# Optimization experiments

Hardware: AMD Instinct MI355X
Metric: run time of the kernel (lower is better)

## Reference

```python
import jax, jax.numpy as jnp
import numpy as np

POSE_DIM, H_DIM, LATENT_DIM, NUM_LAYERS = 96, 32, 16, 2
BATCH, OBS_LEN, PRED_LEN = 16384, 16, 25


def setup_inputs() -> dict:
    key = jax.random.key(0)
    ks = jax.random.split(key, 16)
    s = 0.1
    inp = {
        "obs_s": jax.random.normal(ks[0], (OBS_LEN, BATCH, POSE_DIM), jnp.float32),
        "latent": jax.random.normal(ks[1], (BATCH, LATENT_DIM), jnp.float32),
        "pred_len": PRED_LEN,
        # FC: latent_dim -> h_dim
        "W_fc": jax.random.normal(ks[2], (H_DIM, LATENT_DIM), jnp.float32) * s,
        "b_fc": jnp.zeros((H_DIM,), jnp.float32),
        # LSTM layer 0 (input pose_dim), PyTorch gate order i,f,g,o
        "W_ih0": jax.random.normal(ks[3], (4 * H_DIM, POSE_DIM), jnp.float32) * s,
        "W_hh0": jax.random.normal(ks[4], (4 * H_DIM, H_DIM), jnp.float32) * s,
        "b_ih0": jax.random.normal(ks[5], (4 * H_DIM,), jnp.float32) * s,
        "b_hh0": jax.random.normal(ks[6], (4 * H_DIM,), jnp.float32) * s,
        # LSTM layer 1 (input h_dim)
        "W_ih1": jax.random.normal(ks[7], (4 * H_DIM, H_DIM), jnp.float32) * s,
        "W_hh1": jax.random.normal(ks[8], (4 * H_DIM, H_DIM), jnp.float32) * s,
        "b_ih1": jax.random.normal(ks[9], (4 * H_DIM,), jnp.float32) * s,
        "b_hh1": jax.random.normal(ks[10], (4 * H_DIM,), jnp.float32) * s,
        # mlp: h_dim -> pose_dim
        "W_mlp": jax.random.normal(ks[11], (POSE_DIM, H_DIM), jnp.float32) * s,
        "b_mlp": jnp.zeros((POSE_DIM,), jnp.float32),
    }
    return inp


def _lstm_cell(x, h, c, W_ih, W_hh, b):
    # x: [B, in], h/c: [B, H]; gates in PyTorch order i, f, g, o
    gates = x @ W_ih.T + h @ W_hh.T + b
    i, f, g, o = jnp.split(gates, 4, axis=-1)
    c_new = jax.nn.sigmoid(f) * c + jax.nn.sigmoid(i) * jnp.tanh(g)
    h_new = jax.nn.sigmoid(o) * jnp.tanh(c_new)
    return h_new, c_new


def reference(obs_s, latent, pred_len, W_fc, b_fc,
              W_ih0, W_hh0, b_ih0, b_hh0,
              W_ih1, W_hh1, b_ih1, b_hh1,
              W_mlp, b_mlp):
    batch = obs_s.shape[1]
    h_init = latent @ W_fc.T + b_fc                    # [B, H] -> both layers
    c0 = jnp.zeros((batch, H_DIM), obs_s.dtype)
    b0 = b_ih0 + b_hh0
    b1 = b_ih1 + b_hh1

    def step(carry, _):
        last, h0, c0_, h1, c1_ = carry
        h0, c0_ = _lstm_cell(last, h0, c0_, W_ih0, W_hh0, b0)
        h1, c1_ = _lstm_cell(h0, h1, c1_, W_ih1, W_hh1, b1)
        curr = h1 @ W_mlp.T + b_mlp                    # [B, pose_dim]
        return (curr, h0, c0_, h1, c1_), curr

    init = (obs_s[-1], h_init, c0, h_init, c0)
    _, preds = jax.lax.scan(step, init, None, length=pred_len)
    return preds  # [pred_len, B, pose_dim]
```

## Files before the change

### kernel.cpp

```cpp
#include <hip/hip_runtime.h>


#define PRED 25
#define BATCH 16384
#define ET    32
#define XROW  192
#define HROW  128
#define LROW  64

typedef unsigned short u16;
typedef unsigned int   u32;
typedef __attribute__((ext_vector_type(8))) short bf16x8;
typedef __attribute__((ext_vector_type(4))) float f32x4;

#define LOG2E  1.44269504088896340736f
#define LOG2E2 2.88539008177792681472f

#define BARRIER_NOVM() asm volatile("s_waitcnt lgkmcnt(0)\ns_barrier" ::: "memory")

__device__ __forceinline__ float rcp_(float x){ return __builtin_amdgcn_rcpf(x); }
__device__ __forceinline__ float ex2(float x){ return __builtin_amdgcn_exp2f(x); }
__device__ __forceinline__ float sigm2(float xp){ return rcp_(1.0f + ex2(-xp)); }
__device__ __forceinline__ float tanh2(float xp){ return 1.0f - 2.0f*rcp_(ex2(xp) + 1.0f); }

__device__ __forceinline__ u16 f2b(float f){
  u32 i = __float_as_uint(f);
  i += 0x7FFFu + ((i >> 16) & 1u);
  return (u16)(i >> 16);
}
__device__ __forceinline__ float b2f(u16 u){ return __uint_as_float(((u32)u) << 16); }

struct __align__(16) SM {
  u16 xh[2][16*XROW];
  u16 hh[2][16*HROW];
  u16 h1lo[2][16*LROW];
};

__device__ __forceinline__ int swx(int e, int k){ return e*XROW + (k ^ ((e&7)<<3)); }
__device__ __forceinline__ int swh(int e, int k){ return e*HROW + (k ^ ((e&7)<<3)); }
__device__ __forceinline__ int swl(int e, int k){ return e*LROW + (k ^ ((e&7)<<3)); }

__device__ __forceinline__ bf16x8 pack8s(const float* src, float s){
  union { bf16x8 v; u16 h[8]; } fr;
  #pragma unroll
  for (int j = 0; j < 8; ++j) fr.h[j] = f2b(src[j]*s);
  return fr.v;
}

extern "C" __global__ __launch_bounds__(128, 1)
void decoder_kernel(const float* __restrict__ obs,  const float* __restrict__ lat,
                    const float* __restrict__ Wfc,  const float* __restrict__ bfc,
                    const float* __restrict__ Wih0, const float* __restrict__ Whh0,
                    const float* __restrict__ bih0, const float* __restrict__ bhh0,
                    const float* __restrict__ Wih1, const float* __restrict__ Whh1,
                    const float* __restrict__ bih1, const float* __restrict__ bhh1,
                    const float* __restrict__ Wmlp, const float* __restrict__ bmlp,
                    float* __restrict__ out)
{
  __shared__ SM sm;
  const int tid = threadIdx.x;
  const int ebase = blockIdx.x * ET;
  const int mh = tid >> 6;
  const int l  = tid & 63;
  const int lr = l & 15;
  const int kq = l >> 4;

  {
    int e = tid >> 2, c0 = (tid & 3)*24;
    int s = e >> 4, er = e & 15;
    const float* src = obs + ((size_t)(15*BATCH) + ebase + e)*96 + c0;
    #pragma unroll
    for (int j = 0; j < 12; ++j){
      float2 v = *(const float2*)(src + 2*j);
      u32 pk = (u32)f2b(v.x) | ((u32)f2b(v.y) << 16);
      *(u32*)&sm.xh[s][swx(er, c0 + 2*j)] = pk;
    }
  }
  {
    int u = tid & 31, e8 = (tid >> 5)*8;
    const float* wf = Wfc + u*16;
    float bb = bfc[u];
    #pragma unroll
    for (int r = 0; r < 8; ++r){
      int e = e8 + r, s = e >> 4, er = e & 15;
      const float* lp = lat + (size_t)(ebase + e)*16;
      float a = bb;
      #pragma unroll
      for (int j = 0; j < 16; ++j) a = fmaf(wf[j], lp[j], a);
      u16 hb = f2b(a);
      sm.xh[s][swx(er, 96 + u)] = hb;
      sm.hh[s][swh(er, 32 + u)] = hb;
    }
  }

  bf16x8 aw0[4][4];
  #pragma unroll
  for (int i = 0; i < 4; ++i){
    int vg = (mh*4 + i)*16 + lr;
    int g  = (vg & 3)*32 + (vg >> 2);
    float sc = ((vg & 3) == 2) ? LOG2E2 : LOG2E;
    #pragma unroll
    for (int c = 0; c < 4; ++c){
      int k = c*32 + kq*8;
      const float* src = (k < 96) ? (Wih0 + g*96 + k) : (Whh0 + g*32 + (k - 96));
      aw0[i][c] = pack8s(src, sc);
    }
  }
  bf16x8 aw1[4][2];
  #pragma unroll
  for (int i = 0; i < 4; ++i){
    int vg = (mh*4 + i)*16 + lr;
    int g  = (vg & 3)*32 + (vg >> 2);
    float sc = ((vg & 3) == 2) ? LOG2E2 : LOG2E;
    #pragma unroll
    for (int c = 0; c < 2; ++c){
      int k = c*32 + kq*8;
      const float* src = (k < 32) ? (Wih1 + g*32 + k) : (Whh1 + g*32 + (k - 32));
      aw1[i][c] = pack8s(src, sc);
    }
  }
  bf16x8 awm[3];
  #pragma unroll
  for (int i = 0; i < 3; ++i){
    int o = (mh*3 + i)*16 + lr;
    awm[i] = pack8s(Wmlp + o*32 + kq*8, 1.0f);
  }

  f32x4 bias0v[4], bias1v[4];
  #pragma unroll
  for (int i = 0; i < 4; ++i){
    int u = (mh*4 + i)*4 + kq;
    #pragma unroll
    for (int r = 0; r < 4; ++r){
      int g = r*32 + u;
      float sc = (r == 2) ? LOG2E2 : LOG2E;
      bias0v[i][r] = (bih0[g] + bhh0[g])*sc;
      bias1v[i][r] = (bih1[g] + bhh1[g])*sc;
    }
  }
  f32x4 biasmv[3];
  #pragma unroll
  for (int i = 0; i < 3; ++i){
    int o0 = (mh*3 + i)*16 + kq*4;
    #pragma unroll
    for (int r = 0; r < 4; ++r) biasmv[i][r] = bmlp[o0 + r];
  }

  float c0s[2][4] = {{0,0,0,0},{0,0,0,0}};
  float c1s[2][4] = {{0,0,0,0},{0,0,0,0}};

  __syncthreads();

  f32x4 am[2][3];

  for (int t = 0; t < PRED; ++t){
    const int p = t & 1;
    f32x4 g0[2][4];
    #pragma unroll
    for (int s = 0; s < 2; ++s){
      bf16x8 bx0 = *(const bf16x8*)&sm.xh[s][swx(lr, 0*32 + kq*8)];
      bf16x8 bx1 = *(const bf16x8*)&sm.xh[s][swx(lr, 1*32 + kq*8)];
      bf16x8 bx2 = *(const bf16x8*)&sm.xh[s][swx(lr, 2*32 + kq*8)];
      bf16x8 bx3 = *(const bf16x8*)&sm.xh[s][swx(lr, 96 + 32*p + kq*8)];
      #pragma unroll
      for (int i = 0; i < 4; ++i){
        f32x4 a = bias0v[i];
        a = __builtin_amdgcn_mfma_f32_16x16x32_bf16(aw0[i][0], bx0, a, 0, 0, 0);
        a = __builtin_amdgcn_mfma_f32_16x16x32_bf16(aw0[i][1], bx1, a, 0, 0, 0);
        a = __builtin_amdgcn_mfma_f32_16x16x32_bf16(aw0[i][2], bx2, a, 0, 0, 0);
        a = __builtin_amdgcn_mfma_f32_16x16x32_bf16(aw0[i][3], bx3, a, 0, 0, 0);
        g0[s][i] = a;
      }
    }
    #pragma unroll
    for (int s = 0; s < 2; ++s)
      #pragma unroll
      for (int i = 0; i < 4; ++i){
        float ig = sigm2(g0[s][i][0]);
        float fg = sigm2(g0[s][i][1]);
        float gg = tanh2(g0[s][i][2]);
        float og = sigm2(g0[s][i][3]);
        float cn = fmaf(fg, c0s[s][i], ig*gg);
        c0s[s][i] = cn;
        u16 hb = f2b(og * tanh2(cn*LOG2E2));
        int u = (mh*4 + i)*4 + kq;
        sm.xh[s][swx(lr, 96 + 32*(p^1) + u)] = hb;
        sm.hh[s][swh(lr, u)] = hb;
      }
    BARRIER_NOVM();
    f32x4 g1[2][4];
    #pragma unroll
    for (int s = 0; s < 2; ++s){
      bf16x8 bh0 = *(const bf16x8*)&sm.hh[s][swh(lr, kq*8)];
      bf16x8 bh1 = *(const bf16x8*)&sm.hh[s][swh(lr, 32 + 32*p + kq*8)];
      #pragma unroll
      for (int i = 0; i < 4; ++i){
        f32x4 a = bias1v[i];
        a = __builtin_amdgcn_mfma_f32_16x16x32_bf16(aw1[i][0], bh0, a, 0, 0, 0);
        a = __builtin_amdgcn_mfma_f32_16x16x32_bf16(aw1[i][1], bh1, a, 0, 0, 0);
        g1[s][i] = a;
      }
    }
    #pragma unroll
    for (int s = 0; s < 2; ++s)
      #pragma unroll
      for (int i = 0; i < 4; ++i){
        float ig = sigm2(g1[s][i][0]);
        float fg = sigm2(g1[s][i][1]);
        float gg = tanh2(g1[s][i][2]);
        float og = sigm2(g1[s][i][3]);
        float cn = fmaf(fg, c1s[s][i], ig*gg);
        c1s[s][i] = cn;
        float h1 = og * tanh2(cn*LOG2E2);
        u16 hi = f2b(h1);
        u16 lo = f2b(h1 - b2f(hi));
        int u = (mh*4 + i)*4 + kq;
        sm.hh[s][swh(lr, 32 + 32*(p^1) + u)] = hi;
        sm.h1lo[s][swl(lr, u)] = lo;
      }
    BARRIER_NOVM();
    #pragma unroll
    for (int s = 0; s < 2; ++s){
      bf16x8 bmh = *(const bf16x8*)&sm.hh[s][swh(lr, 32 + 32*(p^1) + kq*8)];
      bf16x8 bml = *(const bf16x8*)&sm.h1lo[s][swl(lr, kq*8)];
      #pragma unroll
      for (int i = 0; i < 3; ++i){
        f32x4 a = biasmv[i];
        a = __builtin_amdgcn_mfma_f32_16x16x32_bf16(awm[i], bmh, a, 0, 0, 0);
        a = __builtin_amdgcn_mfma_f32_16x16x32_bf16(awm[i], bml, a, 0, 0, 0);
        am[s][i] = a;
        int o0 = (mh*3 + i)*16 + kq*4;
        u32 pk01 = (u32)f2b(a[0]) | ((u32)f2b(a[1]) << 16);
        u32 pk23 = (u32)f2b(a[2]) | ((u32)f2b(a[3]) << 16);
        *(u32*)&sm.xh[s][swx(lr, o0)]     = pk01;
        *(u32*)&sm.xh[s][swx(lr, o0 + 2)] = pk23;
      }
    }
    BARRIER_NOVM();
    #pragma unroll
    for (int s = 0; s < 2; ++s){
      float* outb = out + (size_t)t*BATCH*96 + (size_t)(ebase + s*16 + lr)*96;
      #pragma unroll
      for (int i = 0; i < 3; ++i){
        int o0 = (mh*3 + i)*16 + kq*4;
        *(f32x4*)(outb + o0) = am[s][i];
      }
    }
  }
}

extern "C" void kernel_launch(void* const* d_in, const int* in_sizes, int n_in,
                              void* d_out, int out_size, void* d_ws, size_t ws_size,
                              hipStream_t stream){
  decoder_kernel<<<dim3(BATCH/ET), dim3(128), 0, stream>>>(
      (const float*)d_in[0],  (const float*)d_in[1],
      (const float*)d_in[3],  (const float*)d_in[4],
      (const float*)d_in[5],  (const float*)d_in[6],
      (const float*)d_in[7],  (const float*)d_in[8],
      (const float*)d_in[9],  (const float*)d_in[10],
      (const float*)d_in[11], (const float*)d_in[12],
      (const float*)d_in[13], (const float*)d_in[14],
      (float*)d_out);
}
```

Baseline: 79.10 us.

## Double batch tile per block and split gate tiles across four waves

```diff
diff --git a/kernel.cpp b/kernel.cpp
--- a/kernel.cpp
+++ b/kernel.cpp
@@ -3,7 +3,7 @@
 
 #define PRED 25
 #define BATCH 16384
-#define ET    32
+#define ET    64
 #define XROW  192
 #define HROW  128
 #define LROW  64
@@ -31,9 +31,9 @@
 __device__ __forceinline__ float b2f(u16 u){ return __uint_as_float(((u32)u) << 16); }
 
 struct __align__(16) SM {
-  u16 xh[2][16*XROW];
-  u16 hh[2][16*HROW];
-  u16 h1lo[2][16*LROW];
+  u16 xh[4][16*XROW];
+  u16 hh[4][16*HROW];
+  u16 h1lo[4][16*LROW];
 };
 
 __device__ __forceinline__ int swx(int e, int k){ return e*XROW + (k ^ ((e&7)<<3)); }
@@ -47,7 +47,7 @@
   return fr.v;
 }
 
-extern "C" __global__ __launch_bounds__(128, 1)
+extern "C" __global__ __launch_bounds__(256, 1)
 void decoder_kernel(const float* __restrict__ obs,  const float* __restrict__ lat,
                     const float* __restrict__ Wfc,  const float* __restrict__ bfc,
                     const float* __restrict__ Wih0, const float* __restrict__ Whh0,
@@ -64,6 +64,7 @@
   const int l  = tid & 63;
   const int lr = l & 15;
   const int kq = l >> 4;
+  const bool nt2 = (mh < 2);
 
   {
     int e = tid >> 2, c0 = (tid & 3)*24;
@@ -93,10 +94,10 @@
     }
   }
 
-  bf16x8 aw0[4][4];
-  #pragma unroll
-  for (int i = 0; i < 4; ++i){
-    int vg = (mh*4 + i)*16 + lr;
+  bf16x8 aw0[2][4];
+  #pragma unroll
+  for (int i = 0; i < 2; ++i){
+    int vg = (mh*2 + i)*16 + lr;
     int g  = (vg & 3)*32 + (vg >> 2);
     float sc = ((vg & 3) == 2) ? LOG2E2 : LOG2E;
     #pragma unroll
@@ -106,10 +107,10 @@
       aw0[i][c] = pack8s(src, sc);
     }
   }
-  bf16x8 aw1[4][2];
-  #pragma unroll
-  for (int i = 0; i < 4; ++i){
-    int vg = (mh*4 + i)*16 + lr;
+  bf16x8 aw1[2][2];
+  #pragma unroll
+  for (int i = 0; i < 2; ++i){
+    int vg = (mh*2 + i)*16 + lr;
     int g  = (vg & 3)*32 + (vg >> 2);
     float sc = ((vg & 3) == 2) ? LOG2E2 : LOG2E;
     #pragma unroll
@@ -119,17 +120,24 @@
       aw1[i][c] = pack8s(src, sc);
     }
   }
-  bf16x8 awm[3];
-  #pragma unroll
-  for (int i = 0; i < 3; ++i){
-    int o = (mh*3 + i)*16 + lr;
-    awm[i] = pack8s(Wmlp + o*32 + kq*8, 1.0f);
-  }
-
-  f32x4 bias0v[4], bias1v[4];
-  #pragma unroll
-  for (int i = 0; i < 4; ++i){
-    int u = (mh*4 + i)*4 + kq;
+  bf16x8 awm[2];
+  f32x4 biasmv[2];
+  #pragma unroll
+  for (int it = 0; it < 2; ++it){
+    int tm = mh + it*4;
+    if (it == 0 || nt2){
+      int o = tm*16 + lr;
+      awm[it] = pack8s(Wmlp + o*32 + kq*8, 1.0f);
+      int o0 = tm*16 + kq*4;
+      #pragma unroll
+      for (int r = 0; r < 4; ++r) biasmv[it][r] = bmlp[o0 + r];
+    }
+  }
+
+  f32x4 bias0v[2], bias1v[2];
+  #pragma unroll
+  for (int i = 0; i < 2; ++i){
+    int u = (mh*2 + i)*4 + kq;
     #pragma unroll
     for (int r = 0; r < 4; ++r){
       int g = r*32 + u;
@@ -138,32 +146,25 @@
       bias1v[i][r] = (bih1[g] + bhh1[g])*sc;
     }
   }
-  f32x4 biasmv[3];
-  #pragma unroll
-  for (int i = 0; i < 3; ++i){
-    int o0 = (mh*3 + i)*16 + kq*4;
-    #pragma unroll
-    for (int r = 0; r < 4; ++r) biasmv[i][r] = bmlp[o0 + r];
-  }
-
-  float c0s[2][4] = {{0,0,0,0},{0,0,0,0}};
-  float c1s[2][4] = {{0,0,0,0},{0,0,0,0}};
+
+  float c0s[4][2] = {{0,0},{0,0},{0,0},{0,0}};
+  float c1s[4][2] = {{0,0},{0,0},{0,0},{0,0}};
 
   __syncthreads();
 
-  f32x4 am[2][3];
+  f32x4 am[4][2];
 
   for (int t = 0; t < PRED; ++t){
     const int p = t & 1;
-    f32x4 g0[2][4];
-    #pragma unroll
-    for (int s = 0; s < 2; ++s){
+    f32x4 g0[4][2];
+    #pragma unroll
+    for (int s = 0; s < 4; ++s){
       bf16x8 bx0 = *(const bf16x8*)&sm.xh[s][swx(lr, 0*32 + kq*8)];
       bf16x8 bx1 = *(const bf16x8*)&sm.xh[s][swx(lr, 1*32 + kq*8)];
       bf16x8 bx2 = *(const bf16x8*)&sm.xh[s][swx(lr, 2*32 + kq*8)];
       bf16x8 bx3 = *(const bf16x8*)&sm.xh[s][swx(lr, 96 + 32*p + kq*8)];
       #pragma unroll
-      for (int i = 0; i < 4; ++i){
+      for (int i = 0; i < 2; ++i){
         f32x4 a = bias0v[i];
         a = __builtin_amdgcn_mfma_f32_16x16x32_bf16(aw0[i][0], bx0, a, 0, 0, 0);
         a = __builtin_amdgcn_mfma_f32_16x16x32_bf16(aw0[i][1], bx1, a, 0, 0, 0);
@@ -173,9 +174,9 @@
       }
     }
     #pragma unroll
-    for (int s = 0; s < 2; ++s)
-      #pragma unroll
-      for (int i = 0; i < 4; ++i){
+    for (int s = 0; s < 4; ++s)
+      #pragma unroll
+      for (int i = 0; i < 2; ++i){
         float ig = sigm2(g0[s][i][0]);
         float fg = sigm2(g0[s][i][1]);
         float gg = tanh2(g0[s][i][2]);
@@ -183,18 +184,18 @@
         float cn = fmaf(fg, c0s[s][i], ig*gg);
         c0s[s][i] = cn;
         u16 hb = f2b(og * tanh2(cn*LOG2E2));
-        int u = (mh*4 + i)*4 + kq;
+        int u = (mh*2 + i)*4 + kq;
         sm.xh[s][swx(lr, 96 + 32*(p^1) + u)] = hb;
         sm.hh[s][swh(lr, u)] = hb;
       }
     BARRIER_NOVM();
-    f32x4 g1[2][4];
-    #pragma unroll
-    for (int s = 0; s < 2; ++s){
+    f32x4 g1[4][2];
+    #pragma unroll
+    for (int s = 0; s < 4; ++s){
       bf16x8 bh0 = *(const bf16x8*)&sm.hh[s][swh(lr, kq*8)];
       bf16x8 bh1 = *(const bf16x8*)&sm.hh[s][swh(lr, 32 + 32*p + kq*8)];
       #pragma unroll
-      for (int i = 0; i < 4; ++i){
+      for (int i = 0; i < 2; ++i){
         f32x4 a = bias1v[i];
         a = __builtin_amdgcn_mfma_f32_16x16x32_bf16(aw1[i][0], bh0, a, 0, 0, 0);
         a = __builtin_amdgcn_mfma_f32_16x16x32_bf16(aw1[i][1], bh1, a, 0, 0, 0);
@@ -202,9 +203,9 @@
       }
     }
     #pragma unroll
-    for (int s = 0; s < 2; ++s)
-      #pragma unroll
-      for (int i = 0; i < 4; ++i){
+    for (int s = 0; s < 4; ++s)
+      #pragma unroll
+      for (int i = 0; i < 2; ++i){
         float ig = sigm2(g1[s][i][0]);
         float fg = sigm2(g1[s][i][1]);
         float gg = tanh2(g1[s][i][2]);
@@ -214,36 +215,41 @@
         float h1 = og * tanh2(cn*LOG2E2);
         u16 hi = f2b(h1);
         u16 lo = f2b(h1 - b2f(hi));
-        int u = (mh*4 + i)*4 + kq;
+        int u = (mh*2 + i)*4 + kq;
         sm.hh[s][swh(lr, 32 + 32*(p^1) + u)] = hi;
         sm.h1lo[s][swl(lr, u)] = lo;
       }
     BARRIER_NOVM();
     #pragma unroll
-    for (int s = 0; s < 2; ++s){
+    for (int s = 0; s < 4; ++s){
       bf16x8 bmh = *(const bf16x8*)&sm.hh[s][swh(lr, 32 + 32*(p^1) + kq*8)];
       bf16x8 bml = *(const bf16x8*)&sm.h1lo[s][swl(lr, kq*8)];
       #pragma unroll
-      for (int i = 0; i < 3; ++i){
-        f32x4 a = biasmv[i];
-        a = __builtin_amdgcn_mfma_f32_16x16x32_bf16(awm[i], bmh, a, 0, 0, 0);
-        a = __builtin_amdgcn_mfma_f32_16x16x32_bf16(awm[i], bml, a, 0, 0, 0);
-        am[s][i] = a;
-        int o0 = (mh*3 + i)*16 + kq*4;
-        u32 pk01 = (u32)f2b(a[0]) | ((u32)f2b(a[1]) << 16);
-        u32 pk23 = (u32)f2b(a[2]) | ((u32)f2b(a[3]) << 16);
-        *(u32*)&sm.xh[s][swx(lr, o0)]     = pk01;
-        *(u32*)&sm.xh[s][swx(lr, o0 + 2)] = pk23;
+      for (int it = 0; it < 2; ++it){
+        if (it == 0 || nt2){
+          int tm = mh + it*4;
+          f32x4 a = biasmv[it];
+          a = __builtin_amdgcn_mfma_f32_16x16x32_bf16(awm[it], bmh, a, 0, 0, 0);
+          a = __builtin_amdgcn_mfma_f32_16x16x32_bf16(awm[it], bml, a, 0, 0, 0);
+          am[s][it] = a;
+          int o0 = tm*16 + kq*4;
+          u32 pk01 = (u32)f2b(a[0]) | ((u32)f2b(a[1]) << 16);
+          u32 pk23 = (u32)f2b(a[2]) | ((u32)f2b(a[3]) << 16);
+          *(u32*)&sm.xh[s][swx(lr, o0)]     = pk01;
+          *(u32*)&sm.xh[s][swx(lr, o0 + 2)] = pk23;
+        }
       }
     }
     BARRIER_NOVM();
     #pragma unroll
-    for (int s = 0; s < 2; ++s){
+    for (int s = 0; s < 4; ++s){
       float* outb = out + (size_t)t*BATCH*96 + (size_t)(ebase + s*16 + lr)*96;
       #pragma unroll
-      for (int i = 0; i < 3; ++i){
-        int o0 = (mh*3 + i)*16 + kq*4;
-        *(f32x4*)(outb + o0) = am[s][i];
+      for (int it = 0; it < 2; ++it){
+        if (it == 0 || nt2){
+          int tm = mh + it*4;
+          *(f32x4*)(outb + tm*16 + kq*4) = am[s][it];
+        }
       }
     }
   }
@@ -252,7 +258,7 @@
 extern "C" void kernel_launch(void* const* d_in, const int* in_sizes, int n_in,
                               void* d_out, int out_size, void* d_ws, size_t ws_size,
                               hipStream_t stream){
-  decoder_kernel<<<dim3(BATCH/ET), dim3(128), 0, stream>>>(
+  decoder_kernel<<<dim3(BATCH/ET), dim3(256), 0, stream>>>(
       (const float*)d_in[0],  (const float*)d_in[1],
       (const float*)d_in[3],  (const float*)d_in[4],
       (const float*)d_in[5],  (const float*)d_in[6],
```

Result: slower. 91.91 us (+16.2%).
